# Optimization experiments

Measured on AMD Instinct MI355X. Metric: run time of the kernel, lower is better.

## Reference

```python
import jax, jax.numpy as jnp
import numpy as np

H = 1024
F = 4096  # base_ffn_dim = hidden * 4
WIDTHS = [256, 512]  # adapters; idx 2 -> width==hidden -> identity
EPS = 1e-5


def _xavier(key, fan_in, fan_out, gain):
    a = gain * np.sqrt(6.0 / (fan_in + fan_out))
    return jax.random.uniform(key, (fan_in, fan_out), jnp.float32, -a, a)


def _layernorm(x, g, b):
    mu = jnp.mean(x, axis=-1, keepdims=True)
    var = jnp.var(x, axis=-1, keepdims=True)
    return (x - mu) * jax.lax.rsqrt(var + EPS) * g + b


def setup_inputs() -> dict:
    key = jax.random.key(0)
    ks = jax.random.split(key, 12)
    g = 1.0 / np.sqrt(2.0)
    B, S = 4, 2048
    return {
        "x": jax.random.normal(ks[0], (B, S, H), jnp.float32),
        "width_multiplier": jax.random.uniform(ks[1], (B, S, 1), jnp.float32),
        "width_idx": jax.random.randint(ks[2], (B, S), 0, 3, jnp.int32),
        "ln_in_g": jnp.ones((H,), jnp.float32),
        "ln_in_b": jnp.zeros((H,), jnp.float32),
        "W1": _xavier(ks[3], H, F, g),
        "b1": jnp.zeros((F,), jnp.float32),
        "ln_h_g": jnp.ones((F,), jnp.float32),
        "ln_h_b": jnp.zeros((F,), jnp.float32),
        "W2": _xavier(ks[4], F, H, g),
        "b2": jnp.zeros((H,), jnp.float32),
        "a256_w1": _xavier(ks[5], H, 256, g),
        "a256_b1": jnp.zeros((256,), jnp.float32),
        "a256_w2": _xavier(ks[6], 256, H, g),
        "a256_b2": jnp.zeros((H,), jnp.float32),
        "a512_w1": _xavier(ks[7], H, 512, g),
        "a512_b1": jnp.zeros((512,), jnp.float32),
        "a512_w2": _xavier(ks[8], 512, H, g),
        "a512_b2": jnp.zeros((H,), jnp.float32),
    }


def reference(x, width_multiplier, width_idx,
              ln_in_g, ln_in_b, W1, b1, ln_h_g, ln_h_b, W2, b2,
              a256_w1, a256_b1, a256_w2, a256_b2,
              a512_w1, a512_b1, a512_w2, a512_b2):
    gelu = lambda t: jax.nn.gelu(t, approximate=False)  # torch nn.GELU exact
    x_norm = _layernorm(x, ln_in_g, ln_in_b)
    # base FFN path
    h = gelu(jnp.einsum("bsh,hf->bsf", x_norm, W1) + b1)
    h = _layernorm(h, ln_h_g, ln_h_b)
    base = jnp.einsum("bsf,fh->bsh", h, W2) + b2
    # width adapters (routed per token by width_idx)
    ad0 = jnp.einsum("bsw,wh->bsh", gelu(jnp.einsum("bsh,hw->bsw", x_norm, a256_w1) + a256_b1), a256_w2) + a256_b2
    ad1 = jnp.einsum("bsw,wh->bsh", gelu(jnp.einsum("bsh,hw->bsw", x_norm, a512_w1) + a512_b1), a512_w2) + a512_b2
    idx = width_idx[..., None]
    adaptive = jnp.where(idx == 0, ad0, jnp.where(idx == 1, ad1, x_norm))
    return base * width_multiplier + adaptive * (1.0 - width_multiplier)
```

## Files before the change

kernel.cpp:

```cpp
#include <hip/hip_runtime.h>
#include <cstdint>
#include <cstddef>

typedef unsigned short u16x8 __attribute__((ext_vector_type(8)));
typedef unsigned short u16x4 __attribute__((ext_vector_type(4)));
typedef __bf16 bf16x8 __attribute__((ext_vector_type(8)));
typedef float f32x4 __attribute__((ext_vector_type(4)));

__device__ __forceinline__ float b2f(unsigned short u) {
    union { unsigned int i; float f; } v;
    v.i = ((unsigned int)u) << 16;
    return v.f;
}

__device__ __forceinline__ unsigned short f2b(float f) {
    union { float f; unsigned int i; } v;
    v.f = f;
    unsigned int x = v.i;
    unsigned int lsb = (x >> 16) & 1u;
    x += 0x7FFFu + lsb;
    return (unsigned short)(x >> 16);
}

__device__ __forceinline__ float gelu_exact(float x) {
    return 0.5f * x * (1.0f + erff(x * 0.70710678118654752f));
}

__device__ __forceinline__ void ld_lds16(const unsigned short* g, unsigned short* l) {
    __builtin_amdgcn_global_load_lds(
        (const __attribute__((address_space(1))) void*)g,
        (__attribute__((address_space(3))) void*)l, 16, 0, 0);
}


__device__ __forceinline__ void transp_body(const float* __restrict__ in,
                                            unsigned short* __restrict__ out,
                                            int R, int C, int ldout,
                                            const float* __restrict__ scale,
                                            int bx, int by) {
    __shared__ float tile[32][33];
    const int tx = threadIdx.x & 31;
    const int ty = threadIdx.x >> 5;
    int x = bx * 32 + tx;
    int y0 = by * 32;
    for (int k = 0; k < 32; k += 8)
        tile[ty + k][tx] = in[(size_t)(y0 + ty + k) * C + x];
    __syncthreads();
    int ox = y0 + tx;
    int oy = bx * 32;
    float sc = scale ? scale[ox] : 1.0f;
    for (int k = 0; k < 32; k += 8)
        out[(size_t)(oy + ty + k) * ldout + ox] = f2b(tile[tx][ty + k] * sc);
}

__device__ __forceinline__ void c01_partial_body(const float* __restrict__ W2,
                                                 const float* __restrict__ g,
                                                 const float* __restrict__ b,
                                                 float* __restrict__ pc0,
                                                 float* __restrict__ pc1,
                                                 int N, int kc, int nb) {
    int n = (nb << 8) + threadIdx.x;
    int k0 = kc << 8;
    float p0 = 0.f, p1 = 0.f;
    for (int k = k0; k < k0 + 256; ++k) {
        float w = W2[(size_t)k * N + n];
        p0 += b[k] * w;
        p1 += g[k] * w;
    }
    pc0[kc * 1024 + n] = p0;
    pc1[kc * 1024 + n] = p1;
}

__device__ __forceinline__ void ln1024_body(const float* __restrict__ in,
                                            unsigned short* __restrict__ out,
                                            const float* __restrict__ g,
                                            const float* __restrict__ b,
                                            int row) {
    const int t = threadIdx.x;
    f32x4 v = ((const f32x4*)(in + (size_t)row * 1024))[t];
    float s = v[0] + v[1] + v[2] + v[3];
    float s2 = v[0] * v[0] + v[1] * v[1] + v[2] * v[2] + v[3] * v[3];
#pragma unroll
    for (int o = 32; o > 0; o >>= 1) {
        s  += __shfl_down(s, o, 64);
        s2 += __shfl_down(s2, o, 64);
    }
    __shared__ float red[8];
    int lane = t & 63, w = t >> 6;
    if (lane == 0) { red[w] = s; red[4 + w] = s2; }
    __syncthreads();
    if (t == 0) {
        red[0] = red[0] + red[1] + red[2] + red[3];
        red[4] = red[4] + red[5] + red[6] + red[7];
    }
    __syncthreads();
    const float inv_n = 1.0f / 1024.0f;
    float mu = red[0] * inv_n;
    float var = red[4] * inv_n - mu * mu;
    float rs = rsqrtf(var + 1e-5f);
    f32x4 gv = ((const f32x4*)g)[t];
    f32x4 bv = ((const f32x4*)b)[t];
    u16x4 ov;
#pragma unroll
    for (int r = 0; r < 4; ++r) ov[r] = f2b((v[r] - mu) * rs * gv[r] + bv[r]);
    ((u16x4*)(out + (size_t)row * 1024))[t] = ov;
}

template <int EPI>
__device__ __forceinline__ void gemm_body(
    unsigned short (*As)[128 * 32], unsigned short (*Bs)[128 * 32],
    int fid, int nbx, int nby,
    const unsigned short* __restrict__ A, int lda,
    const unsigned short* __restrict__ BT, int ldb,
    const float* __restrict__ bias, unsigned short* __restrict__ Cb,
    float* __restrict__ Cf, int N, int K,
    const int* __restrict__ idx,
    const float* __restrict__ wm,
    const unsigned short* __restrict__ adaptive,
    const unsigned short* __restrict__ xn,
    const float* __restrict__ c1v,
    const float* __restrict__ rstat,
    float* __restrict__ ps, float* __restrict__ pq) {
    const int t = threadIdx.x;

    int id = fid;
    const int nwg = nbx * nby;
    if ((nwg & 7) == 0) {
        const int cpx = nwg >> 3;
        id = (id & 7) * cpx + (id >> 3);
    }
    const int bx = id % nbx;
    const int by = id / nbx;
    const int m0 = by * 128;
    const int n0 = bx * 128;

    const int lane = t & 63;
    const int wid = t >> 6;

    const int srow = lane >> 2;
    const int sch  = (lane & 3) ^ (srow & 3);
    const int scol = sch << 3;

    const int wr = (wid >> 1) << 6;
    const int wc = (wid & 1) << 6;
    const int ml = lane & 15;
    const int q = lane >> 4;
    const int qsw = ((q ^ (ml & 3)) << 3);

    f32x4 acc[4][4];
#pragma unroll
    for (int i = 0; i < 4; ++i)
#pragma unroll
        for (int j = 0; j < 4; ++j)
#pragma unroll
            for (int r = 0; r < 4; ++r) acc[i][j][r] = 0.0f;

    const int nk = K >> 5;

#define STAGE(KT, BUF)                                                          \
    {                                                                           \
        _Pragma("unroll")                                                       \
        for (int hh = 0; hh < 2; ++hh) {                                        \
            int rbase = wid * 32 + hh * 16;                                     \
            int row = rbase + srow;                                             \
            ld_lds16(A  + (size_t)(m0 + row) * lda + (KT) * 32 + scol,          \
                     &As[BUF][rbase * 32]);                                     \
            ld_lds16(BT + (size_t)(n0 + row) * ldb + (KT) * 32 + scol,          \
                     &Bs[BUF][rbase * 32]);                                     \
        }                                                                       \
    }

    STAGE(0, 0);
    for (int kt = 0; kt < nk; ++kt) {
        const int cur = kt & 1;
        __syncthreads();
        if (kt + 1 < nk) STAGE(kt + 1, cur ^ 1);

        bf16x8 af[4], bf[4];
#pragma unroll
        for (int i = 0; i < 4; ++i)
            af[i] = *(const bf16x8*)(&As[cur][(wr + i * 16 + ml) * 32 + qsw]);
#pragma unroll
        for (int j = 0; j < 4; ++j)
            bf[j] = *(const bf16x8*)(&Bs[cur][(wc + j * 16 + ml) * 32 + qsw]);
#pragma unroll
        for (int i = 0; i < 4; ++i)
#pragma unroll
            for (int j = 0; j < 4; ++j)
                acc[i][j] = __builtin_amdgcn_mfma_f32_16x16x32_bf16(af[i], bf[j], acc[i][j], 0, 0, 0);
    }
#undef STAGE

#pragma unroll
    for (int i = 0; i < 4; ++i) {
        float rsv[4], rmv[4], wv[4];
        int idv[4];
        float rsum[4], rqs[4];
        if (EPI == 0) {
#pragma unroll
            for (int r = 0; r < 4; ++r) { rsum[r] = 0.f; rqs[r] = 0.f; }
        }
        if (EPI != 0) {
#pragma unroll
            for (int r = 0; r < 4; ++r) {
                int row = m0 + wr + i * 16 + q * 4 + r;
                idv[r] = idx[row];
                if (EPI == 2) {
                    wv[r] = wm[row];
                    rsv[r] = rstat[2 * (size_t)row];
                    rmv[r] = rstat[2 * (size_t)row + 1];
                }
            }
        }
#pragma unroll
        for (int j = 0; j < 4; ++j) {
            int col = n0 + wc + j * 16 + ml;
            float bv = bias[col];
            float bv1 = (EPI == 4) ? bias[1024 + col] : 0.0f;
            float c1c = (EPI == 2) ? c1v[col] : 0.0f;
#pragma unroll
            for (int r = 0; r < 4; ++r) {
                int row = m0 + wr + i * 16 + q * 4 + r;
                size_t off = (size_t)row * N + col;
                if (EPI == 0) {
                    float g = gelu_exact(acc[i][j][r] + bv);
                    Cb[off] = f2b(g);
                    rsum[r] += g;
                    rqs[r] += g * g;
                } else if (EPI == 3) {
                    bool act = (col < 256) ? (idv[r] == 0) : (idv[r] == 1);
                    Cb[off] = f2b(act ? gelu_exact(acc[i][j][r] + bv) : 0.0f);
                } else if (EPI == 4) {
                    float bsel = (idv[r] == 1) ? bv1 : bv;
                    Cb[off] = f2b(acc[i][j][r] + bsel);
                } else {
                    float bval = rsv[r] * acc[i][j][r] + bv - rmv[r] * c1c;
                    float a = b2f((idv[r] <= 1) ? adaptive[off] : xn[off]);
                    Cf[off] = bval * wv[r] + a * (1.0f - wv[r]);
                }
            }
        }
        if (EPI == 0) {
#pragma unroll
            for (int r = 0; r < 4; ++r) {
                float s = rsum[r], s2 = rqs[r];
                s  += __shfl_xor(s, 1);  s2 += __shfl_xor(s2, 1);
                s  += __shfl_xor(s, 2);  s2 += __shfl_xor(s2, 2);
                s  += __shfl_xor(s, 4);  s2 += __shfl_xor(s2, 4);
                s  += __shfl_xor(s, 8);  s2 += __shfl_xor(s2, 8);
                if (ml == 0) {
                    int row = m0 + wr + i * 16 + q * 4 + r;
                    size_t pidx = (size_t)row * 64 + ((n0 + wc) >> 6);
                    ps[pidx] = s;
                    pq[pidx] = s2;
                }
            }
        }
    }
}

__global__ __launch_bounds__(256) void mega_prep(
    const float* __restrict__ W1, const float* __restrict__ W2,
    const float* __restrict__ ln_h_g, const float* __restrict__ ln_h_b,
    const float* __restrict__ a256_w1, const float* __restrict__ a512_w1,
    const float* __restrict__ a256_w2, const float* __restrict__ a512_w2,
    const float* __restrict__ a256_b1, const float* __restrict__ a512_b1,
    const float* __restrict__ a256_b2, const float* __restrict__ a512_b2,
    const float* __restrict__ x, const float* __restrict__ ln_in_g,
    const float* __restrict__ ln_in_b,
    unsigned short* __restrict__ W1T, unsigned short* __restrict__ W2T,
    unsigned short* __restrict__ awup, unsigned short* __restrict__ awdT,
    float* __restrict__ ab1, float* __restrict__ b2sel,
    float* __restrict__ pc0, float* __restrict__ pc1,
    unsigned short* __restrict__ xn) {
    const int H = 1024, F = 4096;
    int bid = blockIdx.x;
    if (bid < 4096) {
        transp_body(W1, W1T, H, F, H, nullptr, bid & 127, bid >> 7);
    } else if (bid < 8192) {
        int l = bid - 4096;
        transp_body(W2, W2T, F, H, F, ln_h_g, l & 31, l >> 5);
    } else if (bid < 8448) {
        int l = bid - 8192;
        transp_body(a256_w1, awup, H, 256, H, nullptr, l & 7, l >> 3);
    } else if (bid < 8960) {
        int l = bid - 8448;
        transp_body(a512_w1, awup + (size_t)256 * H, H, 512, H, nullptr, l & 15, l >> 4);
    } else if (bid < 9216) {
        int l = bid - 8960;
        transp_body(a256_w2, awdT, 256, H, 768, nullptr, l & 31, l >> 5);
    } else if (bid < 9728) {
        int l = bid - 9216;
        transp_body(a512_w2, awdT + 256, 512, H, 768, nullptr, l & 31, l >> 5);
    } else if (bid < 9731) {
        int n = (bid - 9728) * 256 + threadIdx.x;
        if (n < 768) ab1[n] = (n < 256) ? a256_b1[n] : a512_b1[n - 256];
    } else if (bid < 9739) {
        int n = (bid - 9731) * 256 + threadIdx.x;
        b2sel[n] = (n < 1024) ? a256_b2[n] : a512_b2[n - 1024];
    } else if (bid < 9803) {
        int l = bid - 9739;
        c01_partial_body(W2, ln_h_g, ln_h_b, pc0, pc1, H, l >> 2, l & 3);
    } else {
        ln1024_body(x, xn, ln_in_g, ln_in_b, bid - 9803);
    }
}

__global__ __launch_bounds__(256) void big1(
    const unsigned short* __restrict__ xn, const unsigned short* __restrict__ W1T,
    const float* __restrict__ b1, unsigned short* __restrict__ h,
    float* __restrict__ ps, float* __restrict__ pq,
    const unsigned short* __restrict__ awup, const float* __restrict__ ab1,
    unsigned short* __restrict__ tt, const int* __restrict__ widx) {
    __shared__ __align__(16) unsigned short As[2][128 * 32];
    __shared__ __align__(16) unsigned short Bs[2][128 * 32];
    int bid = blockIdx.x;
    if (bid < 2048) {
        gemm_body<0>(As, Bs, bid, 32, 64, xn, 1024, W1T, 1024, b1, h,
                     nullptr, 4096, 1024, nullptr, nullptr, nullptr, nullptr,
                     nullptr, nullptr, ps, pq);
    } else {
        gemm_body<3>(As, Bs, bid - 2048, 6, 64, xn, 1024, awup, 1024, ab1, tt,
                     nullptr, 768, 1024, widx, nullptr, nullptr, nullptr,
                     nullptr, nullptr, nullptr, nullptr);
    }
}

__global__ __launch_bounds__(256) void mid_k(
    const unsigned short* __restrict__ tt, const unsigned short* __restrict__ awdT,
    const float* __restrict__ b2sel, unsigned short* __restrict__ adp,
    const int* __restrict__ widx,
    const float* __restrict__ ps, const float* __restrict__ pq,
    float* __restrict__ stats,
    const float* __restrict__ pc0, const float* __restrict__ pc1,
    const float* __restrict__ b2, float* __restrict__ c0b2,
    float* __restrict__ c1) {
    __shared__ __align__(16) unsigned short As[2][128 * 32];
    __shared__ __align__(16) unsigned short Bs[2][128 * 32];
    int bid = blockIdx.x;
    if (bid < 512) {
        gemm_body<4>(As, Bs, bid, 8, 64, tt, 768, awdT, 768, b2sel, adp,
                     nullptr, 1024, 768, widx, nullptr, nullptr, nullptr,
                     nullptr, nullptr, nullptr, nullptr);
    } else if (bid < 544) {
        int row = (bid - 512) * 256 + threadIdx.x;
        float s0 = 0.f, s1 = 0.f;
        const float* pr = ps + (size_t)row * 64;
        const float* qr = pq + (size_t)row * 64;
#pragma unroll
        for (int c = 0; c < 64; ++c) { s0 += pr[c]; s1 += qr[c]; }
        const float inv = 1.0f / 4096.0f;
        float mu = s0 * inv;
        float var = s1 * inv - mu * mu;
        float rs = rsqrtf(var + 1e-5f);
        stats[2 * (size_t)row]     = rs;
        stats[2 * (size_t)row + 1] = rs * mu;
    } else {
        int n = ((bid - 544) << 8) + threadIdx.x;
        float s0 = b2[n], s1 = 0.f;
#pragma unroll
        for (int kc = 0; kc < 16; ++kc) {
            s0 += pc0[kc * 1024 + n];
            s1 += pc1[kc * 1024 + n];
        }
        c0b2[n] = s0;
        c1[n] = s1;
    }
}

__global__ __launch_bounds__(256) void gemm_fin(
    const unsigned short* __restrict__ A, int lda,
    const unsigned short* __restrict__ BT, int ldb,
    const float* __restrict__ bias, float* __restrict__ Cf, int N, int K,
    const int* __restrict__ idx, const float* __restrict__ wm,
    const unsigned short* __restrict__ adaptive,
    const unsigned short* __restrict__ xn,
    const float* __restrict__ c1v, const float* __restrict__ rstat) {
    __shared__ __align__(16) unsigned short As[2][128 * 32];
    __shared__ __align__(16) unsigned short Bs[2][128 * 32];
    gemm_body<2>(As, Bs, blockIdx.y * gridDim.x + blockIdx.x,
                 gridDim.x, gridDim.y, A, lda, BT, ldb, bias, nullptr, Cf, N, K,
                 idx, wm, adaptive, xn, c1v, rstat, nullptr, nullptr);
}

extern "C" void kernel_launch(void* const* d_in, const int* in_sizes, int n_in,
                              void* d_out, int out_size, void* d_ws, size_t ws_size,
                              hipStream_t stream) {
    const float* x       = (const float*)d_in[0];
    const float* wm      = (const float*)d_in[1];
    const int*   widx    = (const int*)d_in[2];
    const float* ln_in_g = (const float*)d_in[3];
    const float* ln_in_b = (const float*)d_in[4];
    const float* W1      = (const float*)d_in[5];
    const float* b1      = (const float*)d_in[6];
    const float* ln_h_g  = (const float*)d_in[7];
    const float* ln_h_b  = (const float*)d_in[8];
    const float* W2      = (const float*)d_in[9];
    const float* b2      = (const float*)d_in[10];
    const float* a256_w1 = (const float*)d_in[11];
    const float* a256_b1 = (const float*)d_in[12];
    const float* a256_w2 = (const float*)d_in[13];
    const float* a256_b2 = (const float*)d_in[14];
    const float* a512_w1 = (const float*)d_in[15];
    const float* a512_b1 = (const float*)d_in[16];
    const float* a512_w2 = (const float*)d_in[17];
    const float* a512_b2 = (const float*)d_in[18];
    float* out = (float*)d_out;

    const int T = 8192, H = 1024, F = 4096;

    unsigned short* ws0   = (unsigned short*)d_ws;
    unsigned short* xn    = ws0;
    unsigned short* h     = xn    + (size_t)T * H;
    unsigned short* tt    = h     + (size_t)T * F;
    unsigned short* adp   = tt    + (size_t)T * 768;
    unsigned short* W1T   = adp   + (size_t)T * H;
    unsigned short* W2T   = W1T   + (size_t)H * F;
    unsigned short* awup  = W2T   + (size_t)F * H;
    unsigned short* awdT  = awup  + (size_t)768 * H;
    float*          ab1   = (float*)(awdT + (size_t)H * 768);
    float*          b2sel = ab1 + 768;
    float*          stats = b2sel + 2048;
    float*          c0b2  = stats + (size_t)T * 2;
    float*          c1    = c0b2 + H;
    float*          pc0   = c1 + H;
    float*          pc1   = pc0 + 16 * 1024;
    float*          ps    = pc1 + 16 * 1024;
    float*          pq    = ps + (size_t)T * 64;

    mega_prep<<<9803 + T, 256, 0, stream>>>(
        W1, W2, ln_h_g, ln_h_b, a256_w1, a512_w1, a256_w2, a512_w2,
        a256_b1, a512_b1, a256_b2, a512_b2, x, ln_in_g, ln_in_b,
        W1T, W2T, awup, awdT, ab1, b2sel, pc0, pc1, xn);

    big1<<<2048 + 384, 256, 0, stream>>>(
        xn, W1T, b1, h, ps, pq, awup, ab1, tt, widx);

    mid_k<<<512 + 32 + 4, 256, 0, stream>>>(
        tt, awdT, b2sel, adp, widx, ps, pq, stats, pc0, pc1, b2, c0b2, c1);

    gemm_fin<<<dim3(H / 128, T / 128), 256, 0, stream>>>(
        h, F, W2T, F, c0b2, out, H, F, widx, wm, adp, xn, c1, stats);
}
```

Before: 444.2 us.

## Compute hidden LayerNorm row stats from stored bf16 h in a separate pass

Removes the fused per-row sum and sum-of-squares reduction from the first GEMM epilogue, along with the partial-sum buffers. Row statistics are now computed by re-reading the bf16 hidden activations in a new kernel that also runs the adapter up-projection. The first GEMM becomes its own launch, which lightens its epilogue but adds an extra launch and a second full read of the 64MB h tensor. Stats now come from the rounded bf16 values rather than fp32, which slightly changes numerics.

```diff
diff --git a/kernel.cpp b/kernel.cpp
--- a/kernel.cpp
+++ b/kernel.cpp
@@ -106,6 +106,38 @@
     ((u16x4*)(out + (size_t)row * 1024))[t] = ov;
 }
 
+__device__ __forceinline__ void rowstats_body(const unsigned short* __restrict__ h,
+                                              float* __restrict__ st, int row) {
+    const int t = threadIdx.x;
+    const u16x8* p = (const u16x8*)(h + (size_t)row * 4096);
+    float s = 0.f, s2 = 0.f;
+#pragma unroll
+    for (int i = 0; i < 2; ++i) {
+        u16x8 v = p[t + (i << 8)];
+#pragma unroll
+        for (int r = 0; r < 8; ++r) { float f = b2f(v[r]); s += f; s2 += f * f; }
+    }
+#pragma unroll
+    for (int o = 32; o > 0; o >>= 1) {
+        s  += __shfl_down(s, o, 64);
+        s2 += __shfl_down(s2, o, 64);
+    }
+    __shared__ float red2[8];
+    int lane = t & 63, w = t >> 6;
+    if (lane == 0) { red2[w] = s; red2[4 + w] = s2; }
+    __syncthreads();
+    if (t == 0) {
+        float ss = red2[0] + red2[1] + red2[2] + red2[3];
+        float qq = red2[4] + red2[5] + red2[6] + red2[7];
+        const float inv = 1.0f / 4096.0f;
+        float mu = ss * inv;
+        float var = qq * inv - mu * mu;
+        float rs = rsqrtf(var + 1e-5f);
+        st[2 * (size_t)row]     = rs;
+        st[2 * (size_t)row + 1] = rs * mu;
+    }
+}
+
 template <int EPI>
 __device__ __forceinline__ void gemm_body(
     unsigned short (*As)[128 * 32], unsigned short (*Bs)[128 * 32],
@@ -119,8 +151,7 @@
     const unsigned short* __restrict__ adaptive,
     const unsigned short* __restrict__ xn,
     const float* __restrict__ c1v,
-    const float* __restrict__ rstat,
-    float* __restrict__ ps, float* __restrict__ pq) {
+    const float* __restrict__ rstat) {
     const int t = threadIdx.x;
 
     int id = fid;
@@ -195,11 +226,6 @@
     for (int i = 0; i < 4; ++i) {
         float rsv[4], rmv[4], wv[4];
         int idv[4];
-        float rsum[4], rqs[4];
-        if (EPI == 0) {
-#pragma unroll
-            for (int r = 0; r < 4; ++r) { rsum[r] = 0.f; rqs[r] = 0.f; }
-        }
         if (EPI != 0) {
 #pragma unroll
             for (int r = 0; r < 4; ++r) {
@@ -223,10 +249,7 @@
                 int row = m0 + wr + i * 16 + q * 4 + r;
                 size_t off = (size_t)row * N + col;
                 if (EPI == 0) {
-                    float g = gelu_exact(acc[i][j][r] + bv);
-                    Cb[off] = f2b(g);
-                    rsum[r] += g;
-                    rqs[r] += g * g;
+                    Cb[off] = f2b(gelu_exact(acc[i][j][r] + bv));
                 } else if (EPI == 3) {
                     bool act = (col < 256) ? (idv[r] == 0) : (idv[r] == 1);
                     Cb[off] = f2b(act ? gelu_exact(acc[i][j][r] + bv) : 0.0f);
@@ -237,22 +260,6 @@
                     float bval = rsv[r] * acc[i][j][r] + bv - rmv[r] * c1c;
                     float a = b2f((idv[r] <= 1) ? adaptive[off] : xn[off]);
                     Cf[off] = bval * wv[r] + a * (1.0f - wv[r]);
-                }
-            }
-        }
-        if (EPI == 0) {
-#pragma unroll
-            for (int r = 0; r < 4; ++r) {
-                float s = rsum[r], s2 = rqs[r];
-                s  += __shfl_xor(s, 1);  s2 += __shfl_xor(s2, 1);
-                s  += __shfl_xor(s, 2);  s2 += __shfl_xor(s2, 2);
-                s  += __shfl_xor(s, 4);  s2 += __shfl_xor(s2, 4);
-                s  += __shfl_xor(s, 8);  s2 += __shfl_xor(s2, 8);
-                if (ml == 0) {
-                    int row = m0 + wr + i * 16 + q * 4 + r;
-                    size_t pidx = (size_t)row * 64 + ((n0 + wc) >> 6);
-                    ps[pidx] = s;
-                    pq[pidx] = s2;
                 }
             }
         }
@@ -306,23 +313,31 @@
     }
 }
 
-__global__ __launch_bounds__(256) void big1(
+__global__ __launch_bounds__(256) void gemm1(
     const unsigned short* __restrict__ xn, const unsigned short* __restrict__ W1T,
-    const float* __restrict__ b1, unsigned short* __restrict__ h,
-    float* __restrict__ ps, float* __restrict__ pq,
-    const unsigned short* __restrict__ awup, const float* __restrict__ ab1,
-    unsigned short* __restrict__ tt, const int* __restrict__ widx) {
+    const float* __restrict__ b1, unsigned short* __restrict__ h) {
+    __shared__ __align__(16) unsigned short As[2][128 * 32];
+    __shared__ __align__(16) unsigned short Bs[2][128 * 32];
+    gemm_body<0>(As, Bs, blockIdx.y * gridDim.x + blockIdx.x,
+                 gridDim.x, gridDim.y, xn, 1024, W1T, 1024, b1, h,
+                 nullptr, 4096, 1024, nullptr, nullptr, nullptr, nullptr,
+                 nullptr, nullptr);
+}
+
+__global__ __launch_bounds__(256) void up_stats(
+    const unsigned short* __restrict__ xn, const unsigned short* __restrict__ awup,
+    const float* __restrict__ ab1, unsigned short* __restrict__ tt,
+    const int* __restrict__ widx,
+    const unsigned short* __restrict__ h, float* __restrict__ st) {
     __shared__ __align__(16) unsigned short As[2][128 * 32];
     __shared__ __align__(16) unsigned short Bs[2][128 * 32];
     int bid = blockIdx.x;
-    if (bid < 2048) {
-        gemm_body<0>(As, Bs, bid, 32, 64, xn, 1024, W1T, 1024, b1, h,
-                     nullptr, 4096, 1024, nullptr, nullptr, nullptr, nullptr,
-                     nullptr, nullptr, ps, pq);
+    if (bid < 384) {
+        gemm_body<3>(As, Bs, bid, 6, 64, xn, 1024, awup, 1024, ab1, tt,
+                     nullptr, 768, 1024, widx, nullptr, nullptr, nullptr,
+                     nullptr, nullptr);
     } else {
-        gemm_body<3>(As, Bs, bid - 2048, 6, 64, xn, 1024, awup, 1024, ab1, tt,
-                     nullptr, 768, 1024, widx, nullptr, nullptr, nullptr,
-                     nullptr, nullptr, nullptr, nullptr);
+        rowstats_body(h, st, bid - 384);
     }
 }
 
@@ -330,8 +345,6 @@
     const unsigned short* __restrict__ tt, const unsigned short* __restrict__ awdT,
     const float* __restrict__ b2sel, unsigned short* __restrict__ adp,
     const int* __restrict__ widx,
-    const float* __restrict__ ps, const float* __restrict__ pq,
-    float* __restrict__ stats,
     const float* __restrict__ pc0, const float* __restrict__ pc1,
     const float* __restrict__ b2, float* __restrict__ c0b2,
     float* __restrict__ c1) {
@@ -341,22 +354,9 @@
     if (bid < 512) {
         gemm_body<4>(As, Bs, bid, 8, 64, tt, 768, awdT, 768, b2sel, adp,
                      nullptr, 1024, 768, widx, nullptr, nullptr, nullptr,
-                     nullptr, nullptr, nullptr, nullptr);
-    } else if (bid < 544) {
-        int row = (bid - 512) * 256 + threadIdx.x;
-        float s0 = 0.f, s1 = 0.f;
-        const float* pr = ps + (size_t)row * 64;
-        const float* qr = pq + (size_t)row * 64;
-#pragma unroll
-        for (int c = 0; c < 64; ++c) { s0 += pr[c]; s1 += qr[c]; }
-        const float inv = 1.0f / 4096.0f;
-        float mu = s0 * inv;
-        float var = s1 * inv - mu * mu;
-        float rs = rsqrtf(var + 1e-5f);
-        stats[2 * (size_t)row]     = rs;
-        stats[2 * (size_t)row + 1] = rs * mu;
+                     nullptr, nullptr);
     } else {
-        int n = ((bid - 544) << 8) + threadIdx.x;
+        int n = ((bid - 512) << 8) + threadIdx.x;
         float s0 = b2[n], s1 = 0.f;
 #pragma unroll
         for (int kc = 0; kc < 16; ++kc) {
@@ -380,7 +380,7 @@
     __shared__ __align__(16) unsigned short Bs[2][128 * 32];
     gemm_body<2>(As, Bs, blockIdx.y * gridDim.x + blockIdx.x,
                  gridDim.x, gridDim.y, A, lda, BT, ldb, bias, nullptr, Cf, N, K,
-                 idx, wm, adaptive, xn, c1v, rstat, nullptr, nullptr);
+                 idx, wm, adaptive, xn, c1v, rstat);
 }
 
 extern "C" void kernel_launch(void* const* d_in, const int* in_sizes, int n_in,
@@ -425,19 +425,18 @@
     float*          c1    = c0b2 + H;
     float*          pc0   = c1 + H;
     float*          pc1   = pc0 + 16 * 1024;
-    float*          ps    = pc1 + 16 * 1024;
-    float*          pq    = ps + (size_t)T * 64;
 
     mega_prep<<<9803 + T, 256, 0, stream>>>(
         W1, W2, ln_h_g, ln_h_b, a256_w1, a512_w1, a256_w2, a512_w2,
         a256_b1, a512_b1, a256_b2, a512_b2, x, ln_in_g, ln_in_b,
         W1T, W2T, awup, awdT, ab1, b2sel, pc0, pc1, xn);
 
-    big1<<<2048 + 384, 256, 0, stream>>>(
-        xn, W1T, b1, h, ps, pq, awup, ab1, tt, widx);
-
-    mid_k<<<512 + 32 + 4, 256, 0, stream>>>(
-        tt, awdT, b2sel, adp, widx, ps, pq, stats, pc0, pc1, b2, c0b2, c1);
+    gemm1<<<dim3(F / 128, T / 128), 256, 0, stream>>>(xn, W1T, b1, h);
+
+    up_stats<<<384 + T, 256, 0, stream>>>(xn, awup, ab1, tt, widx, h, stats);
+
+    mid_k<<<512 + 4, 256, 0, stream>>>(tt, awdT, b2sel, adp, widx,
+                                       pc0, pc1, b2, c0b2, c1);
 
     gemm_fin<<<dim3(H / 128, T / 128), 256, 0, stream>>>(
         h, F, W2T, F, c0b2, out, H, F, widx, wm, adp, xn, c1, stats);
```

Result: faster. 414.8 us (-6.6%).
